# Kernel tuning notes

Measured on AMD Instinct MI355X. Metric: run time of the kernel, lower is better.

The kernel has to match this reference:

```python
import jax, jax.numpy as jnp
import numpy as np

N = 20000      # nodes
E = 320000     # edges (avg degree 16)
F_IN = 512     # post_features
H1, H2 = 1024, 512   # hard-coded GCN hidden widths
F_OUT = 128    # post_embedding
D1, D2 = 152, 48     # hard-coded Dense widths


def setup_inputs() -> dict:
    key = jax.random.key(0)
    ks = jax.random.split(key, 16)
    inp = {
        "x": jax.random.normal(ks[0], (N, F_IN), dtype=jnp.float32),
        "src": jax.random.randint(ks[1], (E,), 0, N, dtype=jnp.int32),
        "dst": jax.random.randint(ks[2], (E,), 0, N, dtype=jnp.int32),
        "edge_weight": jax.random.uniform(ks[3], (E,), dtype=jnp.float32) / 16.0,
        # GCN layer params (xavier-ish scale)
        "W1": jax.random.normal(ks[4], (F_IN, H1), dtype=jnp.float32) * (2.0 / (F_IN + H1)) ** 0.5,
        "b1": jax.random.uniform(ks[5], (H1,), dtype=jnp.float32),
        "W2": jax.random.normal(ks[6], (H1, H2), dtype=jnp.float32) * (2.0 / (H1 + H2)) ** 0.5,
        "b2": jax.random.uniform(ks[7], (H2,), dtype=jnp.float32),
        "W3": jax.random.normal(ks[8], (H2, F_OUT), dtype=jnp.float32) * (2.0 / (H2 + F_OUT)) ** 0.5,
        "b3": jax.random.uniform(ks[9], (F_OUT,), dtype=jnp.float32),
        # Dense head params
        "Wd1": jax.random.normal(ks[10], (F_OUT, D1), dtype=jnp.float32) * (2.0 / F_OUT) ** 0.5,
        "bd1": jnp.zeros((D1,), dtype=jnp.float32),
        "Wd2": jax.random.normal(ks[11], (D1, D2), dtype=jnp.float32) * (2.0 / D1) ** 0.5,
        "bd2": jnp.zeros((D2,), dtype=jnp.float32),
        "Wd3": jax.random.normal(ks[12], (D2, 1), dtype=jnp.float32) * (2.0 / D2) ** 0.5,
        "bd3": jnp.zeros((1,), dtype=jnp.float32),
    }
    return inp


def _spmm(src, dst, w, h, n):
    # out[i] = sum_{e: dst[e]==i} w[e] * h[src[e]]  == A @ h with A sparse COO
    return jax.ops.segment_sum(w[:, None] * h[src], dst, num_segments=n)


def reference(x, src, dst, edge_weight, W1, b1, W2, b2, W3, b3,
              Wd1, bd1, Wd2, bd2, Wd3, bd3):
    n = x.shape[0]
    # GCN layer: x @ W -> spmm(A, .) -> + bias ; tanh between layers 1,2
    h = jnp.tanh(_spmm(src, dst, edge_weight, x @ W1, n) + b1)
    h = jnp.tanh(_spmm(src, dst, edge_weight, h @ W2, n) + b2)
    g = _spmm(src, dst, edge_weight, h @ W3, n) + b3
    # F.dropout treated as identity (deterministic reference / eval mode)
    d = jax.nn.relu(g @ Wd1 + bd1)
    d = jax.nn.relu(d @ Wd2 + bd2)
    d = d @ Wd3 + bd3
    return d
```

## Files before the change

kernel.cpp:

```cpp
#include <hip/hip_runtime.h>
#include <hip/hip_bf16.h>


typedef __attribute__((ext_vector_type(8))) short bf16x8;
typedef __attribute__((ext_vector_type(8))) unsigned short u16x8;
typedef __attribute__((ext_vector_type(4))) float f32x4;
typedef unsigned short u16;

#define MPAD 20096
#define AS1 __attribute__((address_space(1)))
#define AS3 __attribute__((address_space(3)))

__device__ inline u16 f2b(float f) {
  union { float f; unsigned int u; } x; x.f = f;
  unsigned int r = x.u + 0x7FFFu + ((x.u >> 16) & 1u);
  return (u16)(r >> 16);
}
__device__ inline float b2f(u16 u) {
  union { unsigned int u; float f; } x; x.u = ((unsigned int)u) << 16; return x.f;
}
__device__ inline unsigned int cvt_pk_bf16(float lo, float hi) {
  unsigned int r;
  asm("v_cvt_pk_bf16_f32 %0, %1, %2" : "=v"(r) : "v"(lo), "v"(hi));
  return r;
}
__device__ inline float fast_tanh(float x) {
  float cx = fminf(fmaxf(x, -9.f), 9.f);
  float e = __expf(2.f * cx);
  float d = e + 1.f, r;
  asm("v_rcp_f32 %0, %1" : "=v"(r) : "v"(d));
  return (e - 1.f) * r;
}


__device__ inline void wT_tile(const float* __restrict__ W, u16* __restrict__ WT,
                               int K, int N, int KPAD, int NPAD,
                               int bx, int by, float (*tile)[33]) {
  const int kb = by * 32, nb = bx * 32;
  const int tx = threadIdx.x & 31, ty = threadIdx.x >> 5;
  #pragma unroll
  for (int i = 0; i < 4; ++i) {
    int k = kb + ty + i * 8, n = nb + tx;
    tile[ty + i * 8][tx] = (k < K && n < N) ? W[(size_t)k * N + n] : 0.f;
  }
  __syncthreads();
  #pragma unroll
  for (int i = 0; i < 4; ++i) {
    int n = nb + ty + i * 8, k = kb + tx;
    WT[(size_t)n * KPAD + k] = f2b(tile[tx][ty + i * 8]);
  }
}

__global__ __launch_bounds__(256) void prep_all(
    const float* __restrict__ x, u16* __restrict__ xb,
    const float* __restrict__ W1, u16* __restrict__ w1t,
    const float* __restrict__ W2, u16* __restrict__ w2t,
    const float* __restrict__ W3, u16* __restrict__ w3t,
    const float* __restrict__ Wd1, u16* __restrict__ wd1t,
    const float* __restrict__ Wd2, u16* __restrict__ wd2t,
    const float* __restrict__ bd1, float* __restrict__ bd1p,
    const float* __restrict__ bd2, float* __restrict__ bd2p,
    const int* __restrict__ dst, int* __restrict__ cnt1,
    int* __restrict__ cnt2) {
  __shared__ float tile[32][33];
  const int b = blockIdx.x;
  const int tid = threadIdx.x;
  if (b < 512) {
    wT_tile(W1, w1t, 512, 1024, 512, 1024, b % 32, b / 32, tile);
  } else if (b < 1024) {
    int t = b - 512;  wT_tile(W2, w2t, 1024, 512, 1024, 512, t % 16, t / 16, tile);
  } else if (b < 1088) {
    int t = b - 1024; wT_tile(W3, w3t, 512, 128, 512, 128, t % 4, t / 4, tile);
  } else if (b < 1120) {
    int t = b - 1088; wT_tile(Wd1, wd1t, 128, 152, 128, 256, t % 8, t / 8, tile);
  } else if (b < 1152) {
    int t = b - 1120; wT_tile(Wd2, wd2t, 152, 48, 256, 128, t % 4, t / 4, tile);
  } else if (b < 11152) {
    int idx = ((b - 1152) * 256 + tid) * 4;
    if (idx < 20000 * 512) {
      float4 v = *reinterpret_cast<const float4*>(&x[idx]);
      uint2 o;
      o.x = cvt_pk_bf16(v.x, v.y);
      o.y = cvt_pk_bf16(v.z, v.w);
      *reinterpret_cast<uint2*>(&xb[idx]) = o;
    }
  } else if (b == 11152) {
    bd1p[tid] = (tid < 152) ? bd1[tid] : 0.f;
  } else if (b == 11153) {
    if (tid < 128) bd2p[tid] = (tid < 48) ? bd2[tid] : 0.f;
  } else if (b < 12404) {
    int e = (b - 11154) * 256 + tid;
    if (e < 320000) atomicAdd(&cnt1[dst[e]], 1);
  } else {
    int i = (b - 12404) * 256 + tid;
    if (i < 20000) cnt2[i] = 0;
  }
}

__global__ __launch_bounds__(1024) void scan_part(
    const int* __restrict__ in, int* __restrict__ out,
    int* __restrict__ bsum, int n) {
  __shared__ int wsum[16];
  const int lane = threadIdx.x & 63, wv = threadIdx.x >> 6;
  int i = blockIdx.x * 1024 + threadIdx.x;
  int v = (i < n) ? in[i] : 0;
  int s = v;
  #pragma unroll
  for (int off = 1; off < 64; off <<= 1) {
    int t = __shfl_up(s, off, 64);
    if (lane >= off) s += t;
  }
  if (lane == 63) wsum[wv] = s;
  __syncthreads();
  if (wv == 0 && lane < 16) {
    int t = wsum[lane];
    #pragma unroll
    for (int off = 1; off < 16; off <<= 1) {
      int u = __shfl_up(t, off, 64);
      if (lane >= off) t += u;
    }
    wsum[lane] = t;
  }
  __syncthreads();
  int waveoff = (wv == 0) ? 0 : wsum[wv - 1];
  if (i < n) out[i] = waveoff + s - v;
  if (threadIdx.x == 0) bsum[blockIdx.x] = wsum[15];
}
__global__ __launch_bounds__(1024) void scan_fix(
    int* __restrict__ out, const int* __restrict__ bsum, int n, int nb) {
  int b = blockIdx.x;
  int pre = 0, tot = 0;
  for (int j = 0; j < nb; ++j) {
    int v = bsum[j];
    if (j < b) pre += v;
    tot += v;
  }
  int i = b * 1024 + threadIdx.x;
  if (i < n && b > 0) out[i] += pre;
  if (b == 0 && threadIdx.x == 0) out[n] = tot;
}

__global__ __launch_bounds__(256) void scatter_csr(
    const int* __restrict__ dst, const int* __restrict__ src,
    const float* __restrict__ ew, const int* __restrict__ row_ptr,
    int* __restrict__ cnt, unsigned int* __restrict__ csr_pack, int E) {
  int e = blockIdx.x * 256 + threadIdx.x;
  if (e >= E) return;
  int d = dst[e];
  int pos = row_ptr[d] + atomicAdd(&cnt[d], 1);
  csr_pack[pos] = ((unsigned int)f2b(ew[e]) << 16) | (unsigned int)src[e];
}

template <int ACT, bool BIAS, bool OUT_BF16>
__global__ __launch_bounds__(256) void gemm_mfma_db(
    const u16* __restrict__ A, const u16* __restrict__ BT,
    const float* __restrict__ bias, void* __restrict__ C,
    int M, int K, int Nn) {
  __shared__ __align__(16) u16 As[2][128 * 64];
  __shared__ __align__(16) u16 Bs[2][128 * 64];
  const int tid = threadIdx.x;
  const int lane = tid & 63;
  const int wave = tid >> 6;
  const int lo = lane & 15, hi = lane >> 4;
  const int wr = wave >> 1, wc = wave & 1;

  const int gx = gridDim.x;
  const int nwg = gx * gridDim.y;
  const int wg = blockIdx.y * gx + blockIdx.x;
  const int q = nwg >> 3, r = nwg & 7;
  const int xcd = wg & 7, sidx = wg >> 3;
  const int swz = (xcd < r ? xcd * (q + 1) : r * (q + 1) + (xcd - r) * q) + sidx;
  const int row0 = (swz / gx) * 128;
  const int col0 = (swz % gx) * 128;

  const u16* pa[4];
  const u16* pb[4];
  int so[4];
  #pragma unroll
  for (int i = 0; i < 4; ++i) {
    int o = i * 4096 + tid * 16;
    int rr = o >> 7;
    int ke = ((o & 127) >> 1) ^ ((rr & 7) << 3);
    pa[i] = &A[(size_t)(row0 + rr) * K + ke];
    pb[i] = &BT[(size_t)(col0 + rr) * K + ke];
    so[i] = o >> 1;
  }

  const int nk = K >> 6;
  f32x4 acc[4][4] = {};

  auto STAGE = [&](int buf, int kt) {
    const int ko = kt << 6;
    #pragma unroll
    for (int i = 0; i < 4; ++i) {
      __builtin_amdgcn_global_load_lds(
          (const AS1 void*)(pa[i] + ko),
          (AS3 void*)&As[buf][so[i]], 16, 0, 0);
      __builtin_amdgcn_global_load_lds(
          (const AS1 void*)(pb[i] + ko),
          (AS3 void*)&Bs[buf][so[i]], 16, 0, 0);
    }
  };

  STAGE(0, 0);
  STAGE(1, 1);
  asm volatile("s_waitcnt vmcnt(8)" ::: "memory");
  __builtin_amdgcn_s_barrier();

  auto body = [&](int cur, int kt) {
    bf16x8 af[2][4], bfr[2][4];
    #pragma unroll
    for (int ks = 0; ks < 2; ++ks) {
      #pragma unroll
      for (int m = 0; m < 4; ++m) {
        int row = wr * 64 + m * 16 + lo;
        int idx = (row * 64 + ks * 32 + hi * 8) ^ ((row & 7) << 3);
        af[ks][m] = *reinterpret_cast<const bf16x8*>(&As[cur][idx]);
      }
      #pragma unroll
      for (int n = 0; n < 4; ++n) {
        int col = wc * 64 + n * 16 + lo;
        int idx = (col * 64 + ks * 32 + hi * 8) ^ ((col & 7) << 3);
        bfr[ks][n] = *reinterpret_cast<const bf16x8*>(&Bs[cur][idx]);
      }
    }
    __builtin_amdgcn_s_setprio(1);
    #pragma unroll
    for (int ks = 0; ks < 2; ++ks)
      #pragma unroll
      for (int m = 0; m < 4; ++m)
        #pragma unroll
        for (int n = 0; n < 4; ++n)
          acc[m][n] = __builtin_amdgcn_mfma_f32_16x16x32_bf16(
              af[ks][m], bfr[ks][n], acc[m][n], 0, 0, 0);
    __builtin_amdgcn_s_setprio(0);
    asm volatile("s_waitcnt lgkmcnt(0)" ::: "memory");
    __builtin_amdgcn_s_barrier();
    if (kt + 2 < nk) {
      STAGE(cur, kt + 2);
      asm volatile("s_waitcnt vmcnt(8)" ::: "memory");
    } else if (kt + 1 < nk) {
      asm volatile("s_waitcnt vmcnt(0)" ::: "memory");
    }
    __builtin_amdgcn_s_barrier();
  };

  for (int kt = 0; kt < nk; kt += 2) {
    body(0, kt);
    body(1, kt + 1);
  }

  float bv[4];
  if (BIAS) {
    #pragma unroll
    for (int n = 0; n < 4; ++n) bv[n] = bias[col0 + wc * 64 + n * 16 + lo];
  }

  u16* Cb = (u16*)C;
  float* Cf = (float*)C;
  #pragma unroll
  for (int m = 0; m < 4; ++m) {
    int rbase = row0 + wr * 64 + m * 16 + hi * 4;
    #pragma unroll
    for (int n = 0; n < 4; ++n) {
      int c = col0 + wc * 64 + n * 16 + lo;
      float vv[4];
      #pragma unroll
      for (int i = 0; i < 4; ++i) {
        float v = acc[m][n][i];
        if (BIAS) v += bv[n];
        if (ACT == 1) v = fast_tanh(v);
        else if (ACT == 2) v = fmaxf(v, 0.f);
        vv[i] = v;
      }
      if (OUT_BF16) {
        unsigned int r01 = cvt_pk_bf16(vv[0], vv[1]);
        unsigned int r23 = cvt_pk_bf16(vv[2], vv[3]);
        u16* p = Cb + (size_t)rbase * Nn + c;
        p[0]              = (u16)r01;
        p[Nn]             = (u16)(r01 >> 16);
        p[2 * (size_t)Nn] = (u16)r23;
        p[3 * (size_t)Nn] = (u16)(r23 >> 16);
      } else {
        float* p = Cf + (size_t)rbase * Nn + c;
        p[0] = vv[0]; p[Nn] = vv[1];
        p[2 * (size_t)Nn] = vv[2]; p[3 * (size_t)Nn] = vv[3];
      }
    }
  }
}

template <int F, int CHUNKS, int ACT, bool BIAS, bool OUT_BF16>
__global__ __launch_bounds__(256) void spmm_xcd(
    const int* __restrict__ row_ptr, const unsigned int* __restrict__ pack,
    const u16* __restrict__ H, const float* __restrict__ bias,
    void* __restrict__ out, int N) {
  const int ci = blockIdx.x % CHUNKS;
  const int nb = blockIdx.x / CHUNKS;
  const int g = threadIdx.x >> 4;
  const int gl = threadIdx.x & 15;
  const int node = nb * 16 + g;
  if (node >= N) return;
  const int c0 = ci * (F / CHUNKS) + gl * 4;
  const int beg = row_ptr[node], end = row_ptr[node + 1];

  float a0 = 0.f, a1 = 0.f, a2 = 0.f, a3 = 0.f;
  int p = beg;
  for (; p + 3 < end; p += 4) {
    unsigned int k0 = pack[p], k1 = pack[p + 1], k2 = pack[p + 2], k3 = pack[p + 3];
    ushort4 h0 = *reinterpret_cast<const ushort4*>(&H[(size_t)(k0 & 0xFFFFu) * F + c0]);
    ushort4 h1 = *reinterpret_cast<const ushort4*>(&H[(size_t)(k1 & 0xFFFFu) * F + c0]);
    ushort4 h2 = *reinterpret_cast<const ushort4*>(&H[(size_t)(k2 & 0xFFFFu) * F + c0]);
    ushort4 h3 = *reinterpret_cast<const ushort4*>(&H[(size_t)(k3 & 0xFFFFu) * F + c0]);
    float w0 = b2f((u16)(k0 >> 16)), w1 = b2f((u16)(k1 >> 16));
    float w2 = b2f((u16)(k2 >> 16)), w3 = b2f((u16)(k3 >> 16));
    a0 += w0 * b2f(h0.x) + w1 * b2f(h1.x) + w2 * b2f(h2.x) + w3 * b2f(h3.x);
    a1 += w0 * b2f(h0.y) + w1 * b2f(h1.y) + w2 * b2f(h2.y) + w3 * b2f(h3.y);
    a2 += w0 * b2f(h0.z) + w1 * b2f(h1.z) + w2 * b2f(h2.z) + w3 * b2f(h3.z);
    a3 += w0 * b2f(h0.w) + w1 * b2f(h1.w) + w2 * b2f(h2.w) + w3 * b2f(h3.w);
  }
  for (; p < end; ++p) {
    unsigned int k0 = pack[p];
    ushort4 h0 = *reinterpret_cast<const ushort4*>(&H[(size_t)(k0 & 0xFFFFu) * F + c0]);
    float w0 = b2f((u16)(k0 >> 16));
    a0 += w0 * b2f(h0.x); a1 += w0 * b2f(h0.y);
    a2 += w0 * b2f(h0.z); a3 += w0 * b2f(h0.w);
  }
  if (BIAS) {
    a0 += bias[c0]; a1 += bias[c0 + 1]; a2 += bias[c0 + 2]; a3 += bias[c0 + 3];
  }
  if (ACT == 1) {
    a0 = fast_tanh(a0); a1 = fast_tanh(a1);
    a2 = fast_tanh(a2); a3 = fast_tanh(a3);
  }
  if (OUT_BF16) {
    uint2 o;
    o.x = cvt_pk_bf16(a0, a1);
    o.y = cvt_pk_bf16(a2, a3);
    *reinterpret_cast<uint2*>(&((u16*)out)[(size_t)node * F + c0]) = o;
  } else {
    float4 o = make_float4(a0, a1, a2, a3);
    *reinterpret_cast<float4*>(&((float*)out)[(size_t)node * F + c0]) = o;
  }
}

__global__ __launch_bounds__(256) void last_layer_bf16(
    const u16* __restrict__ D2v, const float* __restrict__ W,
    const float* __restrict__ b, float* __restrict__ out,
    int M, int K, int ld) {
  int rr = blockIdx.x * 256 + threadIdx.x;
  if (rr >= M) return;
  float s = b[0];
  const u16* row = &D2v[(size_t)rr * ld];
  #pragma unroll 8
  for (int k = 0; k < 48; ++k) s += b2f(row[k]) * W[k];
  out[rr] = s;
}


extern "C" void kernel_launch(void* const* d_in, const int* in_sizes, int n_in,
                              void* d_out, int out_size, void* d_ws, size_t ws_size,
                              hipStream_t stream) {
  const int N = 20000, E = 320000;
  const int F_IN = 512, H1 = 1024, H2 = 512, F_OUT = 128;
  const int D1P = 256, D2P = 128;

  const float* x    = (const float*)d_in[0];
  const int*   src  = (const int*)d_in[1];
  const int*   dst  = (const int*)d_in[2];
  const float* ew   = (const float*)d_in[3];
  const float* W1   = (const float*)d_in[4];
  const float* b1   = (const float*)d_in[5];
  const float* W2   = (const float*)d_in[6];
  const float* b2   = (const float*)d_in[7];
  const float* W3   = (const float*)d_in[8];
  const float* b3   = (const float*)d_in[9];
  const float* Wd1  = (const float*)d_in[10];
  const float* bd1  = (const float*)d_in[11];
  const float* Wd2  = (const float*)d_in[12];
  const float* bd2  = (const float*)d_in[13];
  const float* Wd3  = (const float*)d_in[14];
  const float* bd3  = (const float*)d_in[15];
  float* out = (float*)d_out;

  size_t off = 0;
  auto alloc = [&](size_t bytes) {
    void* p = (char*)d_ws + off;
    off += (bytes + 255) & ~(size_t)255;
    return p;
  };
  u16* xb   = (u16*)alloc((size_t)MPAD * F_IN * 2);
  u16* ax   = (u16*)alloc((size_t)MPAD * F_IN * 2);
  u16* h1   = (u16*)alloc((size_t)MPAD * H1 * 2);
  u16* w1t  = (u16*)alloc((size_t)H1 * F_IN * 2);
  u16* w2t  = (u16*)alloc((size_t)H2 * H1 * 2);
  u16* w3t  = (u16*)alloc((size_t)F_OUT * H2 * 2);
  u16* wd1t = (u16*)alloc((size_t)D1P * F_OUT * 2);
  u16* wd2t = (u16*)alloc((size_t)D2P * D1P * 2);
  float* bd1p = (float*)alloc((size_t)D1P * 4);
  float* bd2p = (float*)alloc((size_t)D2P * 4);
  int* row_ptr = (int*)alloc((size_t)(N + 1) * 4);
  int* cnt1    = (int*)alloc((size_t)N * 4);
  int* cnt2    = (int*)alloc((size_t)N * 4);
  int* bsum    = (int*)alloc((size_t)32 * 4);
  unsigned int* csr_pack = (unsigned int*)alloc((size_t)E * 4);

  u16* t2 = xb;
  u16* h2 = ax;
  u16* t3 = h1;
  u16* gb = t3 + (size_t)MPAD * F_OUT;
  u16* d1 = gb + (size_t)MPAD * F_OUT;
  u16* d2 = d1 + (size_t)MPAD * D1P;

  auto cdiv = [](int a, int b) { return (a + b - 1) / b; };
  const int NB16 = cdiv(N, 16);

  hipMemsetAsync(cnt1, 0, (size_t)N * 4, stream);
  prep_all<<<12483, 256, 0, stream>>>(x, xb, W1, w1t, W2, w2t, W3, w3t,
                                      Wd1, wd1t, Wd2, wd2t, bd1, bd1p,
                                      bd2, bd2p, dst, cnt1, cnt2);
  scan_part<<<20, 1024, 0, stream>>>(cnt1, row_ptr, bsum, N);
  scan_fix<<<20, 1024, 0, stream>>>(row_ptr, bsum, N, 20);
  scatter_csr<<<cdiv(E, 256), 256, 0, stream>>>(dst, src, ew, row_ptr, cnt2,
                                                csr_pack, E);

  spmm_xcd<512, 8, 0, false, true><<<NB16 * 8, 256, 0, stream>>>(
      row_ptr, csr_pack, xb, nullptr, ax, N);
  gemm_mfma_db<1, true, true><<<dim3(H1 / 128, MPAD / 128), 256, 0, stream>>>(
      ax, w1t, b1, h1, MPAD, F_IN, H1);

  gemm_mfma_db<0, false, true><<<dim3(H2 / 128, MPAD / 128), 256, 0, stream>>>(
      h1, w2t, nullptr, t2, MPAD, H1, H2);
  spmm_xcd<512, 8, 1, true, true><<<NB16 * 8, 256, 0, stream>>>(
      row_ptr, csr_pack, t2, b2, h2, N);

  gemm_mfma_db<0, false, true><<<dim3(F_OUT / 128, MPAD / 128), 256, 0, stream>>>(
      h2, w3t, nullptr, t3, MPAD, H2, F_OUT);
  spmm_xcd<128, 2, 0, true, true><<<NB16 * 2, 256, 0, stream>>>(
      row_ptr, csr_pack, t3, b3, gb, N);

  gemm_mfma_db<2, true, true><<<dim3(D1P / 128, MPAD / 128), 256, 0, stream>>>(
      gb, wd1t, bd1p, d1, MPAD, F_OUT, D1P);
  gemm_mfma_db<2, true, true><<<dim3(D2P / 128, MPAD / 128), 256, 0, stream>>>(
      d1, wd2t, bd2p, d2, MPAD, D1P, D2P);
  last_layer_bf16<<<cdiv(N, 256), 256, 0, stream>>>(d2, Wd3, bd3, out, N, 48, D2P);
}
```

Baseline: 245.3 us.

## Widen SpMM gathers to 16-byte loads and software-prefetch CSR indices

```diff
diff --git a/kernel.cpp b/kernel.cpp
--- a/kernel.cpp
+++ b/kernel.cpp
@@ -3,21 +3,27 @@
 
 
 typedef __attribute__((ext_vector_type(8))) short bf16x8;
-typedef __attribute__((ext_vector_type(8))) unsigned short u16x8;
 typedef __attribute__((ext_vector_type(4))) float f32x4;
 typedef unsigned short u16;
+typedef unsigned int u32;
 
 #define MPAD 20096
 #define AS1 __attribute__((address_space(1)))
 #define AS3 __attribute__((address_space(3)))
 
 __device__ inline u16 f2b(float f) {
-  union { float f; unsigned int u; } x; x.f = f;
-  unsigned int r = x.u + 0x7FFFu + ((x.u >> 16) & 1u);
+  union { float f; u32 u; } x; x.f = f;
+  u32 r = x.u + 0x7FFFu + ((x.u >> 16) & 1u);
   return (u16)(r >> 16);
 }
 __device__ inline float b2f(u16 u) {
-  union { unsigned int u; float f; } x; x.u = ((unsigned int)u) << 16; return x.f;
+  union { u32 u; float f; } x; x.u = ((u32)u) << 16; return x.f;
+}
+__device__ inline float lo_f(u32 u) {
+  union { u32 u; float f; } x; x.u = u << 16; return x.f;
+}
+__device__ inline float hi_f(u32 u) {
+  union { u32 u; float f; } x; x.u = u & 0xFFFF0000u; return x.f;
 }
 __device__ inline unsigned int cvt_pk_bf16(float lo, float hi) {
   unsigned int r;
@@ -143,12 +149,12 @@
 __global__ __launch_bounds__(256) void scatter_csr(
     const int* __restrict__ dst, const int* __restrict__ src,
     const float* __restrict__ ew, const int* __restrict__ row_ptr,
-    int* __restrict__ cnt, unsigned int* __restrict__ csr_pack, int E) {
+    int* __restrict__ cnt, u32* __restrict__ csr_pack, int E) {
   int e = blockIdx.x * 256 + threadIdx.x;
   if (e >= E) return;
   int d = dst[e];
   int pos = row_ptr[d] + atomicAdd(&cnt[d], 1);
-  csr_pack[pos] = ((unsigned int)f2b(ew[e]) << 16) | (unsigned int)src[e];
+  csr_pack[pos] = ((u32)f2b(ew[e]) << 16) | (u32)src[e];
 }
 
 template <int ACT, bool BIAS, bool OUT_BF16>
@@ -291,56 +297,72 @@
 }
 
 template <int F, int CHUNKS, int ACT, bool BIAS, bool OUT_BF16>
-__global__ __launch_bounds__(256) void spmm_xcd(
-    const int* __restrict__ row_ptr, const unsigned int* __restrict__ pack,
+__global__ __launch_bounds__(256) void spmm_pl(
+    const int* __restrict__ row_ptr, const u32* __restrict__ pack,
     const u16* __restrict__ H, const float* __restrict__ bias,
     void* __restrict__ out, int N) {
   const int ci = blockIdx.x % CHUNKS;
   const int nb = blockIdx.x / CHUNKS;
-  const int g = threadIdx.x >> 4;
-  const int gl = threadIdx.x & 15;
-  const int node = nb * 16 + g;
+  const int g = threadIdx.x >> 3;
+  const int gl = threadIdx.x & 7;
+  const int node = nb * 32 + g;
   if (node >= N) return;
-  const int c0 = ci * (F / CHUNKS) + gl * 4;
+  const int c0 = ci * (F / CHUNKS) + gl * 8;
   const int beg = row_ptr[node], end = row_ptr[node + 1];
 
-  float a0 = 0.f, a1 = 0.f, a2 = 0.f, a3 = 0.f;
+  float a[8] = {};
   int p = beg;
-  for (; p + 3 < end; p += 4) {
-    unsigned int k0 = pack[p], k1 = pack[p + 1], k2 = pack[p + 2], k3 = pack[p + 3];
-    ushort4 h0 = *reinterpret_cast<const ushort4*>(&H[(size_t)(k0 & 0xFFFFu) * F + c0]);
-    ushort4 h1 = *reinterpret_cast<const ushort4*>(&H[(size_t)(k1 & 0xFFFFu) * F + c0]);
-    ushort4 h2 = *reinterpret_cast<const ushort4*>(&H[(size_t)(k2 & 0xFFFFu) * F + c0]);
-    ushort4 h3 = *reinterpret_cast<const ushort4*>(&H[(size_t)(k3 & 0xFFFFu) * F + c0]);
-    float w0 = b2f((u16)(k0 >> 16)), w1 = b2f((u16)(k1 >> 16));
-    float w2 = b2f((u16)(k2 >> 16)), w3 = b2f((u16)(k3 >> 16));
-    a0 += w0 * b2f(h0.x) + w1 * b2f(h1.x) + w2 * b2f(h2.x) + w3 * b2f(h3.x);
-    a1 += w0 * b2f(h0.y) + w1 * b2f(h1.y) + w2 * b2f(h2.y) + w3 * b2f(h3.y);
-    a2 += w0 * b2f(h0.z) + w1 * b2f(h1.z) + w2 * b2f(h2.z) + w3 * b2f(h3.z);
-    a3 += w0 * b2f(h0.w) + w1 * b2f(h1.w) + w2 * b2f(h2.w) + w3 * b2f(h3.w);
+  u32 k0 = 0, k1 = 0, k2 = 0, k3 = 0;
+  bool have = (p + 4 <= end);
+  if (have) { k0 = pack[p]; k1 = pack[p + 1]; k2 = pack[p + 2]; k3 = pack[p + 3]; }
+  while (have) {
+    int pn = p + 4;
+    bool haven = (pn + 4 <= end);
+    u32 n0 = 0, n1 = 0, n2 = 0, n3 = 0;
+    if (haven) { n0 = pack[pn]; n1 = pack[pn + 1]; n2 = pack[pn + 2]; n3 = pack[pn + 3]; }
+    uint4 h0 = *reinterpret_cast<const uint4*>(&H[(size_t)(k0 & 0xFFFFu) * F + c0]);
+    uint4 h1 = *reinterpret_cast<const uint4*>(&H[(size_t)(k1 & 0xFFFFu) * F + c0]);
+    uint4 h2 = *reinterpret_cast<const uint4*>(&H[(size_t)(k2 & 0xFFFFu) * F + c0]);
+    uint4 h3 = *reinterpret_cast<const uint4*>(&H[(size_t)(k3 & 0xFFFFu) * F + c0]);
+    float w0 = hi_f(k0), w1 = hi_f(k1), w2 = hi_f(k2), w3 = hi_f(k3);
+    a[0] += w0 * lo_f(h0.x) + w1 * lo_f(h1.x) + w2 * lo_f(h2.x) + w3 * lo_f(h3.x);
+    a[1] += w0 * hi_f(h0.x) + w1 * hi_f(h1.x) + w2 * hi_f(h2.x) + w3 * hi_f(h3.x);
+    a[2] += w0 * lo_f(h0.y) + w1 * lo_f(h1.y) + w2 * lo_f(h2.y) + w3 * lo_f(h3.y);
+    a[3] += w0 * hi_f(h0.y) + w1 * hi_f(h1.y) + w2 * hi_f(h2.y) + w3 * hi_f(h3.y);
+    a[4] += w0 * lo_f(h0.z) + w1 * lo_f(h1.z) + w2 * lo_f(h2.z) + w3 * lo_f(h3.z);
+    a[5] += w0 * hi_f(h0.z) + w1 * hi_f(h1.z) + w2 * hi_f(h2.z) + w3 * hi_f(h3.z);
+    a[6] += w0 * lo_f(h0.w) + w1 * lo_f(h1.w) + w2 * lo_f(h2.w) + w3 * lo_f(h3.w);
+    a[7] += w0 * hi_f(h0.w) + w1 * hi_f(h1.w) + w2 * hi_f(h2.w) + w3 * hi_f(h3.w);
+    p = pn; k0 = n0; k1 = n1; k2 = n2; k3 = n3; have = haven;
   }
   for (; p < end; ++p) {
-    unsigned int k0 = pack[p];
-    ushort4 h0 = *reinterpret_cast<const ushort4*>(&H[(size_t)(k0 & 0xFFFFu) * F + c0]);
-    float w0 = b2f((u16)(k0 >> 16));
-    a0 += w0 * b2f(h0.x); a1 += w0 * b2f(h0.y);
-    a2 += w0 * b2f(h0.z); a3 += w0 * b2f(h0.w);
+    u32 k = pack[p];
+    uint4 hv = *reinterpret_cast<const uint4*>(&H[(size_t)(k & 0xFFFFu) * F + c0]);
+    float wt = hi_f(k);
+    a[0] += wt * lo_f(hv.x); a[1] += wt * hi_f(hv.x);
+    a[2] += wt * lo_f(hv.y); a[3] += wt * hi_f(hv.y);
+    a[4] += wt * lo_f(hv.z); a[5] += wt * hi_f(hv.z);
+    a[6] += wt * lo_f(hv.w); a[7] += wt * hi_f(hv.w);
   }
   if (BIAS) {
-    a0 += bias[c0]; a1 += bias[c0 + 1]; a2 += bias[c0 + 2]; a3 += bias[c0 + 3];
+    #pragma unroll
+    for (int k = 0; k < 8; ++k) a[k] += bias[c0 + k];
   }
   if (ACT == 1) {
-    a0 = fast_tanh(a0); a1 = fast_tanh(a1);
-    a2 = fast_tanh(a2); a3 = fast_tanh(a3);
+    #pragma unroll
+    for (int k = 0; k < 8; ++k) a[k] = fast_tanh(a[k]);
   }
   if (OUT_BF16) {
-    uint2 o;
-    o.x = cvt_pk_bf16(a0, a1);
-    o.y = cvt_pk_bf16(a2, a3);
-    *reinterpret_cast<uint2*>(&((u16*)out)[(size_t)node * F + c0]) = o;
+    uint4 o;
+    o.x = cvt_pk_bf16(a[0], a[1]);
+    o.y = cvt_pk_bf16(a[2], a[3]);
+    o.z = cvt_pk_bf16(a[4], a[5]);
+    o.w = cvt_pk_bf16(a[6], a[7]);
+    *reinterpret_cast<uint4*>(&((u16*)out)[(size_t)node * F + c0]) = o;
   } else {
-    float4 o = make_float4(a0, a1, a2, a3);
-    *reinterpret_cast<float4*>(&((float*)out)[(size_t)node * F + c0]) = o;
+    float* op = &((float*)out)[(size_t)node * F + c0];
+    #pragma unroll
+    for (int k = 0; k < 8; ++k) op[k] = a[k];
   }
 }
 
@@ -403,7 +425,7 @@
   int* cnt1    = (int*)alloc((size_t)N * 4);
   int* cnt2    = (int*)alloc((size_t)N * 4);
   int* bsum    = (int*)alloc((size_t)32 * 4);
-  unsigned int* csr_pack = (unsigned int*)alloc((size_t)E * 4);
+  u32* csr_pack = (u32*)alloc((size_t)E * 4);
 
   u16* t2 = xb;
   u16* h2 = ax;
@@ -413,7 +435,7 @@
   u16* d2 = d1 + (size_t)MPAD * D1P;
 
   auto cdiv = [](int a, int b) { return (a + b - 1) / b; };
-  const int NB16 = cdiv(N, 16);
+  const int NB32 = cdiv(N, 32);
 
   hipMemsetAsync(cnt1, 0, (size_t)N * 4, stream);
   prep_all<<<12483, 256, 0, stream>>>(x, xb, W1, w1t, W2, w2t, W3, w3t,
@@ -424,19 +446,19 @@
   scatter_csr<<<cdiv(E, 256), 256, 0, stream>>>(dst, src, ew, row_ptr, cnt2,
                                                 csr_pack, E);
 
-  spmm_xcd<512, 8, 0, false, true><<<NB16 * 8, 256, 0, stream>>>(
+  spmm_pl<512, 8, 0, false, true><<<NB32 * 8, 256, 0, stream>>>(
       row_ptr, csr_pack, xb, nullptr, ax, N);
   gemm_mfma_db<1, true, true><<<dim3(H1 / 128, MPAD / 128), 256, 0, stream>>>(
       ax, w1t, b1, h1, MPAD, F_IN, H1);
 
   gemm_mfma_db<0, false, true><<<dim3(H2 / 128, MPAD / 128), 256, 0, stream>>>(
       h1, w2t, nullptr, t2, MPAD, H1, H2);
-  spmm_xcd<512, 8, 1, true, true><<<NB16 * 8, 256, 0, stream>>>(
+  spmm_pl<512, 8, 1, true, true><<<NB32 * 8, 256, 0, stream>>>(
       row_ptr, csr_pack, t2, b2, h2, N);
 
   gemm_mfma_db<0, false, true><<<dim3(F_OUT / 128, MPAD / 128), 256, 0, stream>>>(
       h2, w3t, nullptr, t3, MPAD, H2, F_OUT);
-  spmm_xcd<128, 2, 0, true, true><<<NB16 * 2, 256, 0, stream>>>(
+  spmm_pl<128, 2, 0, true, true><<<NB32 * 2, 256, 0, stream>>>(
       row_ptr, csr_pack, t3, b3, gb, N);
 
   gemm_mfma_db<2, true, true><<<dim3(D1P / 128, MPAD / 128), 256, 0, stream>>>(
```

New measurement: 217.7 us. 11.2% less time.
